# Optimization experiments

Measured on AMD Instinct MI355X. Metric: run time of the kernel, lower is better.

Reference implementation:

```python
import jax, jax.numpy as jnp
import numpy as np

N = 1_000_000   # samples
D_IN = 100      # covariate dim (cfg_density[0][0])
H = 64          # hidden dim
NUM_HEADS = 5   # t-bins [0,.2,.4,.6,.8,1.0]


def setup_inputs() -> dict:
    key = jax.random.key(0)
    ks = jax.random.split(key, 17)
    s = 0.05  # param scale for numerical stability (torch init is data-independent anyway)
    return {
        "t": jax.random.uniform(ks[0], (N,), dtype=jnp.float32),
        "x": jax.random.normal(ks[1], (N, D_IN), dtype=jnp.float32),
        # density feature MLP (two Linear+ReLU layers)
        "dW1": jax.random.normal(ks[2], (D_IN, H), dtype=jnp.float32) * s,
        "db1": jax.random.normal(ks[3], (H,), dtype=jnp.float32) * s,
        "dW2": jax.random.normal(ks[4], (H, H), dtype=jnp.float32) * s,
        "db2": jax.random.normal(ks[5], (H,), dtype=jnp.float32) * s,
        # 5 multi-head branches, each 3 Treat_Linear layers (istreat=1 since isenhance=1)
        "hw1": jax.random.normal(ks[6], (NUM_HEADS, H, H), dtype=jnp.float32) * s,
        "htw1": jax.random.normal(ks[7], (NUM_HEADS, H), dtype=jnp.float32) * s,
        "hb1": jax.random.normal(ks[8], (NUM_HEADS, H), dtype=jnp.float32) * s,
        "hw2": jax.random.normal(ks[9], (NUM_HEADS, H, H), dtype=jnp.float32) * s,
        "htw2": jax.random.normal(ks[10], (NUM_HEADS, H), dtype=jnp.float32) * s,
        "hb2": jax.random.normal(ks[11], (NUM_HEADS, H), dtype=jnp.float32) * s,
        "hw3": jax.random.normal(ks[12], (NUM_HEADS, H, 1), dtype=jnp.float32) * s,
        "htw3": jax.random.normal(ks[13], (NUM_HEADS, 1), dtype=jnp.float32) * s,
        "hb3": jax.random.normal(ks[14], (NUM_HEADS, 1), dtype=jnp.float32) * s,
    }


def reference(t, x, dW1, db1, dW2, db2,
              hw1, htw1, hb1, hw2, htw2, hb2, hw3, htw3, hb3):
    # hidden_features: Linear+ReLU, Linear+ReLU
    h = jax.nn.relu(x @ dW1 + db1)        # [N, H]
    h = jax.nn.relu(h @ dW2 + db2)        # [N, H]

    tt = t[:, None]                        # treatment column [N, 1]
    # bin index per row: t in [0.2*q, 0.2*(q+1)); last bin closed at 1.0
    bins = jnp.clip(jnp.floor(t * NUM_HEADS).astype(jnp.int32), 0, NUM_HEADS - 1)

    out = jnp.zeros((x.shape[0], 1), dtype=h.dtype)
    for q in range(NUM_HEADS):  # fixed small set of structurally-distinct heads
        # Treat_Linear layer 1: feat@W + t*tw + b, relu
        a = jax.nn.relu(h @ hw1[q] + tt * htw1[q] + hb1[q])
        # Treat_Linear layer 2
        a = jax.nn.relu(a @ hw2[q] + tt * htw2[q] + hb2[q])
        # last layer: no activation, islastlayer=1
        a = a @ hw3[q] + tt * htw3[q] + hb3[q]   # [N, 1]
        out = out + jnp.where((bins == q)[:, None], a, 0.0)
    return out  # Drnet returns (None, Q); g is None so we return Q
```

## Files before the change

### kernel.cpp

```cpp
#include <hip/hip_runtime.h>

typedef _Float16 f16;
typedef _Float16 f16x8 __attribute__((ext_vector_type(8)));
typedef float f32x16 __attribute__((ext_vector_type(16)));
typedef unsigned long long u64;

#define NB 5
#define DIN 100
#define NT 512
#define GRID 256
#define NWAVES (GRID * 8)

#define FID_W2 14
#define FID_HD 24
#define NFID   (FID_HD + NB * 25)
#define NENT   (NFID * 64)

__global__ __launch_bounds__(256)
void prepack_kernel(const float* __restrict__ dW1, const float* __restrict__ db1,
                    const float* __restrict__ dW2, const float* __restrict__ db2,
                    const float* __restrict__ hw1, const float* __restrict__ htw1, const float* __restrict__ hb1,
                    const float* __restrict__ hw2, const float* __restrict__ htw2, const float* __restrict__ hb2,
                    const float* __restrict__ hw3, const float* __restrict__ htw3, const float* __restrict__ hb3,
                    f16x8* __restrict__ pw)
{
    int E = blockIdx.x * 256 + threadIdx.x;
    if (E >= NENT) return;
    const int lane = E & 63, fid = E >> 6;
    const int hi8 = (lane >> 5) * 8, m = lane & 31;
    f16x8 v;
    if (fid < FID_W2) {
        int ks = fid >> 1, mm = (fid & 1) * 32 + m;
        #pragma unroll
        for (int e = 0; e < 8; ++e) {
            int k = 16 * ks + hi8 + e;
            float val = (k < 100) ? dW1[k * 64 + mm] : (k == 100 ? db1[mm] : 0.f);
            v[e] = (f16)val;
        }
    } else if (fid < FID_HD) {
        int f = fid - FID_W2;
        int ks = f >> 1, mm = (f & 1) * 32 + m;
        #pragma unroll
        for (int e = 0; e < 8; ++e) {
            int k = 16 * ks + hi8 + e;
            float val = (k < 64) ? dW2[k * 64 + mm] : (k == 64 ? db2[mm] : 0.f);
            v[e] = (f16)val;
        }
    } else {
        int f = fid - FID_HD, q = f / 25, r = f % 25;
        if (r < 20) {
            int layer = r / 10, rr = r % 10;
            int ks = rr >> 1, mm = (rr & 1) * 32 + m;
            const float* W = layer ? hw2 : hw1;
            const float* B = layer ? hb2 : hb1;
            const float* T = layer ? htw2 : htw1;
            #pragma unroll
            for (int e = 0; e < 8; ++e) {
                int k = 16 * ks + hi8 + e;
                float val = (k < 64) ? W[q * 4096 + k * 64 + mm]
                          : (k == 64 ? B[q * 64 + mm]
                          : (k == 65 ? T[q * 64 + mm] : 0.f));
                v[e] = (f16)val;
            }
        } else {
            int ks = r - 20;
            #pragma unroll
            for (int e = 0; e < 8; ++e) {
                int k = 16 * ks + hi8 + e;
                float val = 0.f;
                if (m == 0)
                    val = (k < 64) ? hw3[q * 64 + k]
                        : (k == 64 ? hb3[q] : (k == 65 ? htw3[q] : 0.f));
                v[e] = (f16)val;
            }
        }
    }
    pw[E] = v;
}

__device__ __forceinline__ f32x16 mfma32(f16x8 a, f16x8 b, f32x16 c) {
    return __builtin_amdgcn_mfma_f32_32x32x16_f16(a, b, c, 0, 0, 0);
}
__device__ __forceinline__ f32x16 vzero() {
    f32x16 z;
    #pragma unroll
    for (int i = 0; i < 16; ++i) z[i] = 0.f;
    return z;
}
__device__ __forceinline__ unsigned pk2(float a, float b) {
    union { f16 h[2]; unsigned u; } z; z.h[0] = (f16)a; z.h[1] = (f16)b; return z.u;
}
__device__ __forceinline__ f16x8 frag4(unsigned a, unsigned b, unsigned c, unsigned d) {
    union { unsigned u[4]; f16x8 v; } z; z.u[0]=a; z.u[1]=b; z.u[2]=c; z.u[3]=d; return z.v;
}

#define EPIR(W, A) { \
    W[0]=pk2(fmaxf(A[0],0.f), fmaxf(A[1],0.f)); \
    W[1]=pk2(fmaxf(A[2],0.f), fmaxf(A[3],0.f)); \
    W[2]=pk2(fmaxf(A[4],0.f), fmaxf(A[5],0.f)); \
    W[3]=pk2(fmaxf(A[6],0.f), fmaxf(A[7],0.f)); \
    W[4]=pk2(fmaxf(A[8],0.f), fmaxf(A[9],0.f)); \
    W[5]=pk2(fmaxf(A[10],0.f),fmaxf(A[11],0.f)); \
    W[6]=pk2(fmaxf(A[12],0.f),fmaxf(A[13],0.f)); \
    W[7]=pk2(fmaxf(A[14],0.f),fmaxf(A[15],0.f)); }

#define MKB(dst, Wm, jb) { \
    unsigned s0_=__shfl_xor(Wm[jb+0],32,64), s1_=__shfl_xor(Wm[jb+1],32,64); \
    unsigned s2_=__shfl_xor(Wm[jb+2],32,64), s3_=__shfl_xor(Wm[jb+3],32,64); \
    dst = frag4(lo ? Wm[jb+0] : s2_, lo ? Wm[jb+1] : s3_, \
                lo ? s0_ : Wm[jb+2], lo ? s1_ : Wm[jb+3]); }

__global__ __launch_bounds__(NT, 2)
void drnet_main(const float* __restrict__ t, const float* __restrict__ x,
                const f16x8* __restrict__ pw,
                float* __restrict__ out, int N, int NG)
{
    __shared__ __align__(16) f16x8 swts[NENT];
    __shared__ unsigned short ssrt[8][64];
    __shared__ float sstv[8][64];
    __shared__ float sout[8][64];

    const int tid = threadIdx.x;
    const int lane = tid & 63;
    const int wv = tid >> 6;
    const int hi = lane >> 5;
    const int sm = lane & 31;
    const bool lo = (hi == 0);

    for (int p = tid; p < NENT; p += NT)
        ((float4*)swts)[p] = ((const float4*)pw)[p];
    __syncthreads();

    #define TF(fid) swts[(fid)*64 + lane]

    const f16x8 bfb = lo ? frag4(pk2(1.f, 0.f), 0u, 0u, 0u) : frag4(0u, 0u, 0u, 0u);

    auto do_tile = [&](const f16x8* xb, f16x8 bft, int li, int rq, int qlo, int qhiR) {
        if (qlo >= NB) return;
        const int qhi = min(qhiR, NB - 1);

        f32x16 a0 = vzero(), a1 = vzero();
        #pragma unroll
        for (int ks = 0; ks < 7; ++ks) {
            a0 = mfma32(TF(ks*2 + 0), xb[ks], a0);
            a1 = mfma32(TF(ks*2 + 1), xb[ks], a1);
        }
        unsigned WA[8], WB[8];
        EPIR(WA, a0); EPIR(WB, a1);
        f16x8 h0, h1_, h2_, h3_;
        MKB(h0, WA, 0); MKB(h1_, WA, 4); MKB(h2_, WB, 0); MKB(h3_, WB, 4);

        f32x16 c0 = vzero(), c1 = vzero();
        c0 = mfma32(TF(FID_W2+0), h0, c0);  c1 = mfma32(TF(FID_W2+1), h0, c1);
        c0 = mfma32(TF(FID_W2+2), h1_, c0); c1 = mfma32(TF(FID_W2+3), h1_, c1);
        c0 = mfma32(TF(FID_W2+4), h2_, c0); c1 = mfma32(TF(FID_W2+5), h2_, c1);
        c0 = mfma32(TF(FID_W2+6), h3_, c0); c1 = mfma32(TF(FID_W2+7), h3_, c1);
        c0 = mfma32(TF(FID_W2+8), bfb, c0); c1 = mfma32(TF(FID_W2+9), bfb, c1);
        unsigned UA[8], UB[8];
        EPIR(UA, c0); EPIR(UB, c1);
        f16x8 g0, g1, g2, g3;
        MKB(g0, UA, 0); MKB(g1, UA, 4); MKB(g2, UB, 0); MKB(g3, UB, 4);

        #pragma unroll 1
        for (int q = qlo; q <= qhi; ++q) {
            const int hf = FID_HD + q * 25;
            f32x16 d0 = vzero(), d1 = vzero();
            d0 = mfma32(TF(hf+0), g0, d0);  d1 = mfma32(TF(hf+1), g0, d1);
            d0 = mfma32(TF(hf+2), g1, d0);  d1 = mfma32(TF(hf+3), g1, d1);
            d0 = mfma32(TF(hf+4), g2, d0);  d1 = mfma32(TF(hf+5), g2, d1);
            d0 = mfma32(TF(hf+6), g3, d0);  d1 = mfma32(TF(hf+7), g3, d1);
            d0 = mfma32(TF(hf+8), bft, d0); d1 = mfma32(TF(hf+9), bft, d1);
            unsigned VA[8], VB[8];
            EPIR(VA, d0); EPIR(VB, d1);
            f16x8 e0, e1, e2, e3;
            MKB(e0, VA, 0); MKB(e1, VA, 4); MKB(e2, VB, 0); MKB(e3, VB, 4);

            f32x16 f0 = vzero(), f1 = vzero();
            f0 = mfma32(TF(hf+10), e0, f0);  f1 = mfma32(TF(hf+11), e0, f1);
            f0 = mfma32(TF(hf+12), e1, f0);  f1 = mfma32(TF(hf+13), e1, f1);
            f0 = mfma32(TF(hf+14), e2, f0);  f1 = mfma32(TF(hf+15), e2, f1);
            f0 = mfma32(TF(hf+16), e3, f0);  f1 = mfma32(TF(hf+17), e3, f1);
            f0 = mfma32(TF(hf+18), bft, f0); f1 = mfma32(TF(hf+19), bft, f1);
            unsigned YA[8], YB[8];
            EPIR(YA, f0); EPIR(YB, f1);
            f16x8 z0, z1, z2, z3;
            MKB(z0, YA, 0); MKB(z1, YA, 4); MKB(z2, YB, 0); MKB(z3, YB, 4);

            f32x16 o0 = vzero();
            o0 = mfma32(TF(hf+20), z0, o0);
            o0 = mfma32(TF(hf+21), z1, o0);
            o0 = mfma32(TF(hf+22), z2, o0);
            o0 = mfma32(TF(hf+23), z3, o0);
            o0 = mfma32(TF(hf+24), bft, o0);
            if (lo && rq == q)
                sout[wv][li] = o0[0];
        }
    };

    auto sortw = [&](int gn, float tvn) {
        const int i0 = gn * 64 + lane;
        const int qme = (i0 < N) ? min((int)(tvn * 5.0f), NB - 1) : NB;
        const u64 lowm = (1ull << lane) - 1ull;
        int pos = 0;
        #pragma unroll
        for (int b = 0; b <= NB; ++b) {
            u64 mb = __ballot(qme == b);
            int ca = __popcll(mb), cb = __popcll(mb & lowm);
            pos += (b < qme) ? ca : ((b == qme) ? cb : 0);
        }
        ssrt[wv][pos] = (unsigned short)(lane | (qme << 8));
        sstv[wv][pos] = tvn;
        __asm__ volatile("s_waitcnt lgkmcnt(0)" ::: "memory");
    };

    auto issue_x = [&](float4* r, int gn, int li) {
        const float4* xp = (const float4*)(x + (size_t)min(gn * 64 + li, N - 1) * DIN);
        #pragma unroll
        for (int ks = 0; ks < 6; ++ks) { r[2*ks] = xp[4*ks + 2*hi]; r[2*ks+1] = xp[4*ks + 2*hi + 1]; }
        r[12] = lo ? xp[24] : make_float4(0.f, 0.f, 0.f, 0.f);
    };

    auto convert = [&](f16x8* xb, const float4* r) {
        #pragma unroll
        for (int ks = 0; ks < 6; ++ks)
            xb[ks] = frag4(pk2(r[2*ks].x, r[2*ks].y),   pk2(r[2*ks].z, r[2*ks].w),
                           pk2(r[2*ks+1].x, r[2*ks+1].y), pk2(r[2*ks+1].z, r[2*ks+1].w));
        xb[6] = frag4(pk2(r[12].x, r[12].y), pk2(r[12].z, r[12].w),
                      lo ? pk2(1.0f, 0.f) : 0u, 0u);
    };

    const int gw = blockIdx.x * 8 + wv;
    const int S = NWAVES;

    float4 raw0[13], raw1[13];
    float treg = 0.f;
    int g = gw;
    if (g < NG) {
        treg = t[min(g * 64 + lane, N - 1)];
        sortw(g, treg);
        { int li = ssrt[wv][sm] & 63; issue_x(raw0, g, li); }
        { int gn = g + S; treg = (gn < NG) ? t[min(gn * 64 + lane, N - 1)] : 0.f; }
    }

    #pragma unroll 1
    for (; g < NG; g += S) {
        const unsigned short pk0 = ssrt[wv][sm], pk1 = ssrt[wv][32 + sm];
        const int li0 = pk0 & 63, rq0 = pk0 >> 8;
        const int li1 = pk1 & 63, rq1 = pk1 >> 8;
        const float rt0 = sstv[wv][sm], rt1 = sstv[wv][32 + sm];
        const int qlo0 = ssrt[wv][0]  >> 8, qh0 = ssrt[wv][31] >> 8;
        const int qlo1 = ssrt[wv][32] >> 8, qh1 = ssrt[wv][63] >> 8;
        const f16x8 bft0 = lo ? frag4(pk2(1.f, rt0), 0u, 0u, 0u) : frag4(0u, 0u, 0u, 0u);
        const f16x8 bft1 = lo ? frag4(pk2(1.f, rt1), 0u, 0u, 0u) : frag4(0u, 0u, 0u, 0u);

        issue_x(raw1, g, li1);
        f16x8 xb0[7], xb1[7];
        convert(xb0, raw0);
        __builtin_amdgcn_sched_barrier(0);
        do_tile(xb0, bft0, li0, rq0, qlo0, qh0);
        __builtin_amdgcn_sched_barrier(0);

        const bool last = (g + S >= NG);
        if (!last) {
            sortw(g + S, treg);
            { int gn2 = g + 2 * S; treg = (gn2 < NG) ? t[min(gn2 * 64 + lane, N - 1)] : 0.f; }
            { int li = ssrt[wv][sm] & 63; issue_x(raw0, g + S, li); }
            __builtin_amdgcn_sched_barrier(0);
        }
        convert(xb1, raw1);
        do_tile(xb1, bft1, li1, rq1, qlo1, qh1);

        __asm__ volatile("s_waitcnt lgkmcnt(0)" ::: "memory");
        const int ig = g * 64 + lane;
        if (ig < N) out[ig] = sout[wv][lane];
    }
    #undef TF
}

extern "C" void kernel_launch(void* const* d_in, const int* in_sizes, int n_in,
                              void* d_out, int out_size, void* d_ws, size_t ws_size,
                              hipStream_t stream) {
    const float* t    = (const float*)d_in[0];
    const float* x    = (const float*)d_in[1];
    const float* dW1  = (const float*)d_in[2];
    const float* db1  = (const float*)d_in[3];
    const float* dW2  = (const float*)d_in[4];
    const float* db2  = (const float*)d_in[5];
    const float* hw1  = (const float*)d_in[6];
    const float* htw1 = (const float*)d_in[7];
    const float* hb1  = (const float*)d_in[8];
    const float* hw2  = (const float*)d_in[9];
    const float* htw2 = (const float*)d_in[10];
    const float* hb2  = (const float*)d_in[11];
    const float* hw3  = (const float*)d_in[12];
    const float* htw3 = (const float*)d_in[13];
    const float* hb3  = (const float*)d_in[14];
    float* out = (float*)d_out;

    const int N = in_sizes[0];
    const int NG = (N + 63) / 64;
    f16x8* pw = (f16x8*)d_ws;

    prepack_kernel<<<(NENT + 255) / 256, 256, 0, stream>>>(
        dW1, db1, dW2, db2, hw1, htw1, hb1, hw2, htw2, hb2, hw3, htw3, hb3, pw);
    drnet_main<<<GRID, NT, 0, stream>>>(t, x, pw, out, N, NG);
}
```

Baseline: 151.4 us.

## Raise waves per block to twelve with single raw x buffer and nontemporal loads

Grows the block from 8 to 12 waves and asks for 3 blocks per CU. To free registers for that, it merges the two raw x prefetch buffers into one that is converted and then refilled in turn. Per-row t values for the sorted order are now fetched by wave shuffle instead of a shared-memory array, and x and t are read with nontemporal loads. The goal is more latency hiding through higher occupancy. In exchange each wave has less prefetch depth, since every load must land before the next half-tile's convert, so stalls may become exposed.

Result: slower. 220.4 us (+45.6%).

```diff
diff --git a/kernel.cpp b/kernel.cpp
--- a/kernel.cpp
+++ b/kernel.cpp
@@ -3,13 +3,14 @@
 typedef _Float16 f16;
 typedef _Float16 f16x8 __attribute__((ext_vector_type(8)));
 typedef float f32x16 __attribute__((ext_vector_type(16)));
+typedef float f32x4v __attribute__((ext_vector_type(4)));
 typedef unsigned long long u64;
 
 #define NB 5
 #define DIN 100
-#define NT 512
+#define NT 768
 #define GRID 256
-#define NWAVES (GRID * 8)
+#define NWAVES (GRID * 12)
 
 #define FID_W2 14
 #define FID_HD 24
@@ -110,15 +111,14 @@
     dst = frag4(lo ? Wm[jb+0] : s2_, lo ? Wm[jb+1] : s3_, \
                 lo ? s0_ : Wm[jb+2], lo ? s1_ : Wm[jb+3]); }
 
-__global__ __launch_bounds__(NT, 2)
+__global__ __launch_bounds__(NT, 3)
 void drnet_main(const float* __restrict__ t, const float* __restrict__ x,
                 const f16x8* __restrict__ pw,
                 float* __restrict__ out, int N, int NG)
 {
     __shared__ __align__(16) f16x8 swts[NENT];
-    __shared__ unsigned short ssrt[8][64];
-    __shared__ float sstv[8][64];
-    __shared__ float sout[8][64];
+    __shared__ unsigned short ssrt[12][64];
+    __shared__ float sout[12][64];
 
     const int tid = threadIdx.x;
     const int lane = tid & 63;
@@ -209,37 +209,40 @@
             pos += (b < qme) ? ca : ((b == qme) ? cb : 0);
         }
         ssrt[wv][pos] = (unsigned short)(lane | (qme << 8));
-        sstv[wv][pos] = tvn;
         __asm__ volatile("s_waitcnt lgkmcnt(0)" ::: "memory");
     };
 
-    auto issue_x = [&](float4* r, int gn, int li) {
-        const float4* xp = (const float4*)(x + (size_t)min(gn * 64 + li, N - 1) * DIN);
-        #pragma unroll
-        for (int ks = 0; ks < 6; ++ks) { r[2*ks] = xp[4*ks + 2*hi]; r[2*ks+1] = xp[4*ks + 2*hi + 1]; }
-        r[12] = lo ? xp[24] : make_float4(0.f, 0.f, 0.f, 0.f);
+    auto issue_x = [&](f32x4v* r, int gn, int li) {
+        const f32x4v* xp = (const f32x4v*)(x + (size_t)min(gn * 64 + li, N - 1) * DIN);
+        #pragma unroll
+        for (int ks = 0; ks < 6; ++ks) {
+            r[2*ks]   = __builtin_nontemporal_load(xp + 4*ks + 2*hi);
+            r[2*ks+1] = __builtin_nontemporal_load(xp + 4*ks + 2*hi + 1);
+        }
+        if (lo) r[12] = __builtin_nontemporal_load(xp + 24);
+        else    { f32x4v z = {0.f,0.f,0.f,0.f}; r[12] = z; }
     };
 
-    auto convert = [&](f16x8* xb, const float4* r) {
+    auto convert = [&](f16x8* xb, const f32x4v* r) {
         #pragma unroll
         for (int ks = 0; ks < 6; ++ks)
-            xb[ks] = frag4(pk2(r[2*ks].x, r[2*ks].y),   pk2(r[2*ks].z, r[2*ks].w),
-                           pk2(r[2*ks+1].x, r[2*ks+1].y), pk2(r[2*ks+1].z, r[2*ks+1].w));
-        xb[6] = frag4(pk2(r[12].x, r[12].y), pk2(r[12].z, r[12].w),
+            xb[ks] = frag4(pk2(r[2*ks][0], r[2*ks][1]),   pk2(r[2*ks][2], r[2*ks][3]),
+                           pk2(r[2*ks+1][0], r[2*ks+1][1]), pk2(r[2*ks+1][2], r[2*ks+1][3]));
+        xb[6] = frag4(pk2(r[12][0], r[12][1]), pk2(r[12][2], r[12][3]),
                       lo ? pk2(1.0f, 0.f) : 0u, 0u);
     };
 
-    const int gw = blockIdx.x * 8 + wv;
+    const int gw = blockIdx.x * 12 + wv;
     const int S = NWAVES;
 
-    float4 raw0[13], raw1[13];
-    float treg = 0.f;
+    f32x4v raw[13];
+    float tcur = 0.f, treg = 0.f;
     int g = gw;
     if (g < NG) {
-        treg = t[min(g * 64 + lane, N - 1)];
-        sortw(g, treg);
-        { int li = ssrt[wv][sm] & 63; issue_x(raw0, g, li); }
-        { int gn = g + S; treg = (gn < NG) ? t[min(gn * 64 + lane, N - 1)] : 0.f; }
+        tcur = __builtin_nontemporal_load(&t[min(g * 64 + lane, N - 1)]);
+        sortw(g, tcur);
+        { int li = ssrt[wv][sm] & 63; issue_x(raw, g, li); }
+        { int gn = g + S; treg = (gn < NG) ? __builtin_nontemporal_load(&t[min(gn * 64 + lane, N - 1)]) : 0.f; }
     }
 
     #pragma unroll 1
@@ -247,28 +250,33 @@
         const unsigned short pk0 = ssrt[wv][sm], pk1 = ssrt[wv][32 + sm];
         const int li0 = pk0 & 63, rq0 = pk0 >> 8;
         const int li1 = pk1 & 63, rq1 = pk1 >> 8;
-        const float rt0 = sstv[wv][sm], rt1 = sstv[wv][32 + sm];
+        const float rt0 = __shfl(tcur, li0, 64);
+        const float rt1 = __shfl(tcur, li1, 64);
         const int qlo0 = ssrt[wv][0]  >> 8, qh0 = ssrt[wv][31] >> 8;
         const int qlo1 = ssrt[wv][32] >> 8, qh1 = ssrt[wv][63] >> 8;
         const f16x8 bft0 = lo ? frag4(pk2(1.f, rt0), 0u, 0u, 0u) : frag4(0u, 0u, 0u, 0u);
         const f16x8 bft1 = lo ? frag4(pk2(1.f, rt1), 0u, 0u, 0u) : frag4(0u, 0u, 0u, 0u);
 
-        issue_x(raw1, g, li1);
-        f16x8 xb0[7], xb1[7];
-        convert(xb0, raw0);
+        f16x8 xb[7];
+        convert(xb, raw);
+        issue_x(raw, g, li1);
         __builtin_amdgcn_sched_barrier(0);
-        do_tile(xb0, bft0, li0, rq0, qlo0, qh0);
+        do_tile(xb, bft0, li0, rq0, qlo0, qh0);
         __builtin_amdgcn_sched_barrier(0);
 
         const bool last = (g + S >= NG);
         if (!last) {
             sortw(g + S, treg);
-            { int gn2 = g + 2 * S; treg = (gn2 < NG) ? t[min(gn2 * 64 + lane, N - 1)] : 0.f; }
-            { int li = ssrt[wv][sm] & 63; issue_x(raw0, g + S, li); }
-            __builtin_amdgcn_sched_barrier(0);
-        }
-        convert(xb1, raw1);
-        do_tile(xb1, bft1, li1, rq1, qlo1, qh1);
+            tcur = treg;
+            { int gn2 = g + 2 * S; treg = (gn2 < NG) ? __builtin_nontemporal_load(&t[min(gn2 * 64 + lane, N - 1)]) : 0.f; }
+        }
+        convert(xb, raw);
+        if (!last) {
+            int li = ssrt[wv][sm] & 63;
+            issue_x(raw, g + S, li);
+        }
+        __builtin_amdgcn_sched_barrier(0);
+        do_tile(xb, bft1, li1, rq1, qlo1, qh1);
 
         __asm__ volatile("s_waitcnt lgkmcnt(0)" ::: "memory");
         const int ig = g * 64 + lane;
```
